# Kernel tuning notes

Measured on AMD Instinct MI355X. Metric: run time of the kernel, lower is better.

Reference implementation:

```python
import jax, jax.numpy as jnp
import numpy as np

HALT_EPS = 0.1
THRESHOLD = 1.0 - HALT_EPS


def setup_inputs() -> dict:
    key = jax.random.key(0)
    ks = jax.random.split(key, 8)
    bsz, seq_len, d, max_hops = 8, 1024, 1024, 6
    d_ff = 4 * d
    inp = {
        "state": jax.random.normal(ks[0], (bsz, seq_len, d), jnp.float32),
        "time_signal": jax.random.normal(ks[1], (1, seq_len, d), jnp.float32) * 0.02,
        "position_signal": jax.random.normal(ks[2], (1, max_hops, d), jnp.float32) * 0.02,
        "w_p": jax.random.normal(ks[3], (d, 1), jnp.float32) * 0.02,
        "b_p": jnp.ones((1,), jnp.float32),  # p.bias.data.fill_(1.0)
        "W1": jax.random.normal(ks[4], (d, d_ff), jnp.float32) * (1.0 / np.sqrt(d)),
        "b1": jnp.zeros((d_ff,), jnp.float32),
        "W2": jax.random.normal(ks[5], (d_ff, d), jnp.float32) * (1.0 / np.sqrt(d_ff)),
        "b2": jnp.zeros((d,), jnp.float32),
        "max_hops": max_hops,
    }
    return inp


def reference(state, time_signal, position_signal, w_p, b_p, W1, b1, W2, b2, max_hops):
    bsz, seq_len, d = state.shape
    dt = state.dtype
    hp = jnp.zeros((bsz, seq_len), dt)   # halting_probability
    rem = jnp.zeros((bsz, seq_len), dt)  # remainders
    nu = jnp.zeros((bsz, seq_len), dt)   # n_updates
    prev = jnp.zeros_like(state)         # previous_state

    def ffn(x):  # transform(): hidden -> 4*hidden -> ReLU -> hidden
        return jax.nn.relu(x @ W1 + b1) @ W2 + b2

    mh = jnp.asarray(max_hops, dt)
    for step in range(max_hops):
        # emulate the data-dependent early break with a scalar gate
        active = jnp.any((hp < THRESHOLD) & (nu < mh))
        s = state + time_signal[:, :seq_len, :]
        s = s + position_signal[:, step, :][:, None, :]
        p = jax.nn.sigmoid(s @ w_p + b_p)[..., 0]  # [bsz, seq_len]
        sr = (hp < 1.0).astype(dt)                 # still_running
        acc = hp + p * sr
        nh = ((acc > THRESHOLD).astype(dt)) * sr   # new_halted
        sr2 = ((acc <= THRESHOLD).astype(dt)) * sr # still_running (updated)
        hp_n = hp + p * sr2
        rem_n = rem + nh * (1.0 - hp_n)
        hp_n = hp_n + nh * rem_n
        nu_n = nu + sr2 + nh
        uw = (p * sr2 + nh * rem_n)[..., None]     # update_weights
        s_t = ffn(s)
        prev_n = s_t * uw + prev * (1.0 - uw)
        # commit only if the torch loop would not have broken yet
        state = jnp.where(active, s_t, state)
        hp = jnp.where(active, hp_n, hp)
        rem = jnp.where(active, rem_n, rem)
        nu = jnp.where(active, nu_n, nu)
        prev = jnp.where(active, prev_n, prev)
    return prev, (rem, nu)
```

## Files before the change

kernel.cpp:

```cpp
#include <hip/hip_runtime.h>
#include <math.h>

typedef unsigned short u16;
typedef unsigned int u32;
typedef __attribute__((ext_vector_type(8))) short short8;
typedef __attribute__((ext_vector_type(4))) float f32x4;
typedef __attribute__((ext_vector_type(4))) u16 u16x4;

#define BSZ 8
#define SEQ 1024
#define DIM 1024
#define DFF 4096
#define MROWS (BSZ * SEQ)
#define HOPS 6

typedef __attribute__((address_space(3))) u32 as3_u32;
typedef __attribute__((address_space(1))) const u32 as1_u32;
#define GLDS(g, l) __builtin_amdgcn_global_load_lds((as1_u32*)(g), (as3_u32*)(l), 16, 0, 0)

__device__ __forceinline__ u16 bf16_rne(float f) {
  u32 u = __float_as_uint(f);
  u32 r = (u + 0x7FFFu + ((u >> 16) & 1u)) >> 16;
  return (u16)r;
}
__device__ __forceinline__ float bf16_to_f(u16 h) {
  return __uint_as_float(((u32)h) << 16);
}

__global__ __launch_bounds__(256)
void tsplit(const float* __restrict__ W, u16* __restrict__ Th, u16* __restrict__ Tl,
            int K, int N) {
  __shared__ float tile[32][33];
  const int n0 = blockIdx.x * 32, k0 = blockIdx.y * 32;
  const int tx = threadIdx.x & 31, ty = threadIdx.x >> 5;
#pragma unroll
  for (int i = 0; i < 4; ++i)
    tile[ty + 8 * i][tx] = W[(long)(k0 + ty + 8 * i) * N + n0 + tx];
  __syncthreads();
#pragma unroll
  for (int i = 0; i < 4; ++i) {
    float v = tile[tx][ty + 8 * i];
    long idx = (long)(n0 + ty + 8 * i) * K + k0 + tx;
    u16 h = bf16_rne(v);
    Th[idx] = h;
    Tl[idx] = bf16_rne(v - bf16_to_f(h));
  }
}

__global__ __launch_bounds__(256)
void s_act(const float* __restrict__ state, const float* __restrict__ ts,
           const float* __restrict__ ps, const float* __restrict__ wp,
           const float* __restrict__ bp,
           u16* __restrict__ sh, u16* __restrict__ sl,
           float* __restrict__ uwp, float* __restrict__ hp,
           float* __restrict__ rem, float* __restrict__ nu) {
  const int row = blockIdx.x;
  const int t = row & (SEQ - 1);
  const int tid = threadIdx.x;
  const long gbase = (long)row * DIM + tid * 4;
  const int dbase = tid * 4;
  f32x4 sv = *(const f32x4*)(state + gbase);
  f32x4 tv = *(const f32x4*)(ts + (long)t * DIM + dbase);
  f32x4 pv = *(const f32x4*)(ps + dbase);
  f32x4 wv = *(const f32x4*)(wp + dbase);
  float dot = 0.f;
  u16x4 hh, llv;
#pragma unroll
  for (int i = 0; i < 4; ++i) {
    float s = sv[i] + tv[i] + pv[i];
    dot += s * wv[i];
    u16 h = bf16_rne(s);
    hh[i] = h;
    llv[i] = bf16_rne(s - bf16_to_f(h));
  }
  *(u16x4*)(sh + gbase) = hh;
  *(u16x4*)(sl + gbase) = llv;
#pragma unroll
  for (int o = 32; o > 0; o >>= 1) dot += __shfl_down(dot, o);
  __shared__ float red[4];
  if ((tid & 63) == 0) red[tid >> 6] = dot;
  __syncthreads();
  if (tid == 0) {
    float z = red[0] + red[1] + red[2] + red[3] + bp[0];
    float p = 1.0f / (1.0f + expf(-z));
    float h = hp[row], r = rem[row], n = nu[row];
    float sr  = (h < 1.0f) ? 1.0f : 0.0f;
    float a   = h + p * sr;
    float nh  = (a > 0.9f) ? sr : 0.0f;
    float sr2 = (a <= 0.9f) ? sr : 0.0f;
    h = h + p * sr2;
    r = r + nh * (1.0f - h);
    h = h + nh * r;
    n = n + sr2 + nh;
    hp[row] = h; rem[row] = r; nu[row] = n;
    uwp[row] = p * sr2 + nh * r;
  }
}

template <int MODE, int NCOLS>
__global__ __launch_bounds__(512, 2)
void gemm8(const u16* __restrict__ aH, const u16* __restrict__ aL,
           const u16* __restrict__ bH, const u16* __restrict__ bL,
           int ldK, int ntPerSplit,
           const float* __restrict__ bias,
           u16* __restrict__ outH, u16* __restrict__ outL,
           float* __restrict__ parts, int Mrows) {
  __shared__ __align__(16) char lds[131072];
  const int tid = threadIdx.x, lane = tid & 63, wave = tid >> 6;
  const int wm = wave >> 2, wn = wave & 3;

  const int gx = gridDim.x, gy = gridDim.y;
  const int nwg = gx * gy * gridDim.z;
  int id = (blockIdx.z * gy + blockIdx.y) * gx + blockIdx.x;
  int swz = (id & 7) * (nwg >> 3) + (id >> 3);
  const int bx = swz % gx;
  int t1 = swz / gx;
  const int by = t1 % gy, bz = t1 / gy;
  const int m0 = by * 256, n0 = bx * 256;
  const int tile0 = bz * ntPerSplit;
  const int NT = ntPerSplit;
  const int niter = NT >> 1;

  const int l8 = lane >> 3, l7 = lane & 7;
  const int lslot = l7 ^ l8;
  u32 rA[2][2], rB[2][2];
#pragma unroll
  for (int hf = 0; hf < 2; ++hf)
#pragma unroll
    for (int g = 0; g < 2; ++g) {
      rA[hf][g] = (u32)(((m0 + hf * 128 + g * 64 + wave * 8 + l8) * ldK + lslot * 8) * 2);
      rB[hf][g] = (u32)(((n0 + hf * 128 + g * 64 + wave * 8 + l8) * ldK + lslot * 8) * 2);
    }

  auto stage = [&](int T, int hf) {
    const int c = T - (T / 3) * 3;
    const int colb = (T / 3) * 128;
    const int buf = T & 1;
    char* ldsb = &lds[buf * 65536 + (hf >= 2 ? 32768 : 0) + (hf & 1) * 16384 + wave * 1024];
    const u16* pl;
    u32 r0b, r1b;
    if (hf < 2) { pl = (c == 2) ? aL : aH; r0b = rA[hf][0]; r1b = rA[hf][1]; }
    else        { pl = (c == 1) ? bL : bH; r0b = rB[hf - 2][0]; r1b = rB[hf - 2][1]; }
    GLDS((const char*)pl + r0b + colb, ldsb);
    GLDS((const char*)pl + r1b + colb, ldsb + 8192);
  };

  const int fr = lane & 15, kg = lane >> 4;
  const int fb2 = (fr >> 2) & 1;
  const int sks[2] = {fb2 << 6, (fb2 ^ 1) << 6};
  const int laneRC = fr * 128 + ((kg ^ (fr & 3)) << 4);
  const int aBaseH = wm * 16384;
  const int bBaseH = 32768 + (wn >> 1) * 16384 + (wn & 1) * 8192;

  f32x4 acc[8][4];
  const f32x4 fz = {0.f, 0.f, 0.f, 0.f};
#pragma unroll
  for (int m = 0; m < 8; ++m)
#pragma unroll
    for (int n = 0; n < 4; ++n) acc[m][n] = fz;

#define LDS8(off) (*(const short8*)&lds[(off)])

  stage(tile0 + 0, 0); stage(tile0 + 0, 1); stage(tile0 + 0, 2); stage(tile0 + 0, 3);
  stage(tile0 + 1, 0);
  asm volatile("s_waitcnt vmcnt(2)" ::: "memory");
  __builtin_amdgcn_s_barrier();

  for (int it = 0; it < niter; ++it) {
#pragma unroll
    for (int ht = 0; ht < 2; ++ht) {
      const int buf = ht;
      const int abase = buf * 65536 + aBaseH;
      const int bbase = buf * 65536 + bBaseH;
      short8 aF[4][2], bF[4][2];
#pragma unroll
      for (int ph = 0; ph < 4; ++ph) {
        if (ph == 0) {
#pragma unroll
          for (int mf = 0; mf < 4; ++mf) {
            aF[mf][0] = LDS8(abase + mf * 2048 + laneRC + sks[0]);
            aF[mf][1] = LDS8(abase + mf * 2048 + laneRC + sks[1]);
          }
#pragma unroll
          for (int nf = 0; nf < 2; ++nf) {
            bF[nf][0] = LDS8(bbase + nf * 2048 + laneRC + sks[0]);
            bF[nf][1] = LDS8(bbase + nf * 2048 + laneRC + sks[1]);
          }
        } else if (ph == 1) {
#pragma unroll
          for (int nf = 2; nf < 4; ++nf) {
            bF[nf][0] = LDS8(bbase + nf * 2048 + laneRC + sks[0]);
            bF[nf][1] = LDS8(bbase + nf * 2048 + laneRC + sks[1]);
          }
        } else if (ph == 2) {
#pragma unroll
          for (int mf = 0; mf < 4; ++mf) {
            aF[mf][0] = LDS8(abase + (4 + mf) * 2048 + laneRC + sks[0]);
            aF[mf][1] = LDS8(abase + (4 + mf) * 2048 + laneRC + sks[1]);
          }
        }
        {
          const int gp = 8 * it + ht * 4 + ph + 1;
          const int T = (gp + 4) >> 2;
          const int hf = (ht * 4 + ph + 5) & 3;
          if (T < NT) stage(tile0 + T, hf);
        }
        __builtin_amdgcn_s_barrier();
        asm volatile("s_waitcnt lgkmcnt(0)" ::: "memory");
        __builtin_amdgcn_s_setprio(1);
        {
          const int qm = ph >> 1, qn = ph & 1;
#pragma unroll
          for (int mm = 0; mm < 4; ++mm)
#pragma unroll
            for (int nn = 0; nn < 2; ++nn) {
              const int mf = qm * 4 + mm, nf = qn * 2 + nn;
              acc[mf][nf] = __builtin_amdgcn_mfma_f32_16x16x32_bf16(aF[mm][0], bF[nf][0], acc[mf][nf], 0, 0, 0);
              acc[mf][nf] = __builtin_amdgcn_mfma_f32_16x16x32_bf16(aF[mm][1], bF[nf][1], acc[mf][nf], 0, 0, 0);
            }
        }
        __builtin_amdgcn_s_setprio(0);
        if (ph == 3) {
          if (it + 1 == niter) { asm volatile("s_waitcnt vmcnt(0)" ::: "memory"); }
          else                 { asm volatile("s_waitcnt vmcnt(2)" ::: "memory"); }
        }
        __builtin_amdgcn_s_barrier();
      }
    }
  }

  const int orow = m0 + wm * 128 + kg * 4;
  const int ocol = n0 + wn * 64 + fr;
#pragma unroll
  for (int mf = 0; mf < 8; ++mf)
#pragma unroll
    for (int nf = 0; nf < 4; ++nf) {
      const int col = ocol + nf * 16;
      if constexpr (MODE == 0) {
        const float bv = bias[col];
#pragma unroll
        for (int i2 = 0; i2 < 4; ++i2) {
          const int row = orow + mf * 16 + i2;
          float v = fmaxf(acc[mf][nf][i2] + bv, 0.f);
          const size_t idx = (size_t)row * NCOLS + col;
          u16 h = bf16_rne(v);
          outH[idx] = h;
          outL[idx] = bf16_rne(v - bf16_to_f(h));
        }
      } else {
        float* pp = parts + (size_t)bz * Mrows * NCOLS;
#pragma unroll
        for (int i2 = 0; i2 < 4; ++i2) {
          const int row = orow + mf * 16 + i2;
          pp[(size_t)row * NCOLS + col] = acc[mf][nf][i2];
        }
      }
    }
#undef LDS8
}

__global__ __launch_bounds__(256)
void combine(const float* __restrict__ parts, long pstride, int nparts,
             const float* __restrict__ b2, const float* __restrict__ uwp,
             float* __restrict__ prev, float* __restrict__ state, int n4) {
  for (int idx = blockIdx.x * blockDim.x + threadIdx.x; idx < n4;
       idx += gridDim.x * blockDim.x) {
    const int row = idx >> 8, c4 = idx & 255;
    f32x4 a = ((const f32x4*)parts)[idx];
    for (int k = 1; k < nparts; ++k) {
      f32x4 b = *(const f32x4*)(parts + (long)k * pstride + (long)idx * 4);
#pragma unroll
      for (int j = 0; j < 4; ++j) a[j] += b[j];
    }
    f32x4 bv = ((const f32x4*)b2)[c4];
    const float u = uwp[row];
    f32x4 pr = ((const f32x4*)prev)[idx];
    f32x4 s, o;
#pragma unroll
    for (int j = 0; j < 4; ++j) {
      s[j] = a[j] + bv[j];
      o[j] = s[j] * u + pr[j] * (1.0f - u);
    }
    ((f32x4*)prev)[idx] = o;
    ((f32x4*)state)[idx] = s;
  }
}

extern "C" void kernel_launch(void* const* d_in, const int* in_sizes, int n_in,
                              void* d_out, int out_size, void* d_ws, size_t ws_size,
                              hipStream_t stream) {
  (void)in_sizes; (void)n_in;
  float* state     = (float*)d_in[0];
  const float* ts  = (const float*)d_in[1];
  const float* ps  = (const float*)d_in[2];
  const float* wp  = (const float*)d_in[3];
  const float* bp  = (const float*)d_in[4];
  const float* W1  = (const float*)d_in[5];
  const float* b1  = (const float*)d_in[6];
  const float* W2  = (const float*)d_in[7];
  const float* b2  = (const float*)d_in[8];

  float* prev = (float*)d_out;
  float* rem  = prev + (size_t)MROWS * DIM;
  float* nu   = rem + MROWS;

  char* base = (char*)d_ws;
  size_t off = 0;
  auto carve = [&](size_t bytes) -> void* {
    void* p = base + off;
    off += (bytes + 255) & ~(size_t)255;
    return p;
  };
  u16* w1h = (u16*)carve((size_t)DFF * DIM * 2);
  u16* w1l = (u16*)carve((size_t)DFF * DIM * 2);
  u16* w2h = (u16*)carve((size_t)DIM * DFF * 2);
  u16* w2l = (u16*)carve((size_t)DIM * DFF * 2);
  u16* sh  = (u16*)carve((size_t)MROWS * DIM * 2);
  u16* sl  = (u16*)carve((size_t)MROWS * DIM * 2);
  float* uwp = (float*)carve((size_t)MROWS * 4);
  float* hp  = (float*)carve((size_t)MROWS * 4);
  const size_t fixed = off;
  int Ms = MROWS;
  while (Ms > 256 && fixed + (size_t)16384 * DIM * 4 + (size_t)Ms * 16384 > ws_size)
    Ms >>= 1;
  u16* hidh    = (u16*)carve((size_t)Ms * DFF * 2);
  u16* hidl    = (u16*)carve((size_t)Ms * DFF * 2);
  float* parts = (float*)carve((size_t)16384 * DIM * 4);
  const int sk = 16384 / Ms;
  const int ntps = 192 / sk;

  hipMemsetAsync(d_out, 0, (size_t)out_size * 4, stream);
  hipMemsetAsync(hp, 0, (size_t)MROWS * 4, stream);

  tsplit<<<dim3(DFF / 32, DIM / 32), 256, 0, stream>>>(W1, w1h, w1l, DIM, DFF);
  tsplit<<<dim3(DIM / 32, DFF / 32), 256, 0, stream>>>(W2, w2h, w2l, DFF, DIM);

  for (int step = 0; step < HOPS; ++step) {
    s_act<<<MROWS, 256, 0, stream>>>(state, ts, ps + (size_t)step * DIM, wp, bp,
                                     sh, sl, uwp, hp, rem, nu);
    for (int r0 = 0; r0 < MROWS; r0 += Ms) {
      gemm8<0, DFF><<<dim3(DFF / 256, Ms / 256, 1), 512, 0, stream>>>(
          sh + (size_t)r0 * DIM, sl + (size_t)r0 * DIM, w1h, w1l,
          DIM, 48, b1, hidh, hidl, nullptr, Ms);
      gemm8<1, DIM><<<dim3(DIM / 256, Ms / 256, sk), 512, 0, stream>>>(
          hidh, hidl, w2h, w2l,
          DFF, ntps, nullptr, nullptr, nullptr, parts, Ms);
      combine<<<2048, 256, 0, stream>>>(
          parts, (long)Ms * DIM, sk, b2, uwp + r0,
          prev + (size_t)r0 * DIM, state + (size_t)r0 * DIM, Ms * 256);
    }
  }
}
```

Baseline: 2.641 ms.

## Fuse combine into next step's activation kernel and add device-side early-exit gates

When the whole batch fits in one chunk, the split-K reduction, bias, previous-state blend and state update are folded into the next hop's s_act kernel. A separate final combine runs once after the last hop. This removes one full-size pass over state and parts per hop. Each kernel also reads a device-side gate flag, set when any row is still running, and returns early if all rows have halted, which emulates the reference's early break without a host sync. The catch is extra atomic loads at kernel entry; with the given inputs, rows may never all halt, so the gates may never skip anything.

```diff
diff --git a/kernel.cpp b/kernel.cpp
--- a/kernel.cpp
+++ b/kernel.cpp
@@ -26,6 +26,9 @@
 __device__ __forceinline__ float bf16_to_f(u16 h) {
   return __uint_as_float(((u32)h) << 16);
 }
+__device__ __forceinline__ int gchk(const int* g) {
+  return g ? __hip_atomic_load(g, __ATOMIC_RELAXED, __HIP_MEMORY_SCOPE_AGENT) : 1;
+}
 
 __global__ __launch_bounds__(256)
 void tsplit(const float* __restrict__ W, u16* __restrict__ Th, u16* __restrict__ Tl,
@@ -47,19 +50,38 @@
   }
 }
 
+template <int NP>
 __global__ __launch_bounds__(256)
-void s_act(const float* __restrict__ state, const float* __restrict__ ts,
-           const float* __restrict__ ps, const float* __restrict__ wp,
-           const float* __restrict__ bp,
-           u16* __restrict__ sh, u16* __restrict__ sl,
-           float* __restrict__ uwp, float* __restrict__ hp,
-           float* __restrict__ rem, float* __restrict__ nu) {
+void s_act_k(const float* __restrict__ src, long pstride,
+             const float* __restrict__ b2, float* __restrict__ prevO,
+             const float* __restrict__ ts, const float* __restrict__ ps,
+             const float* __restrict__ wp, const float* __restrict__ bp,
+             u16* __restrict__ sh, u16* __restrict__ sl,
+             float* __restrict__ uwp, float* __restrict__ hp,
+             float* __restrict__ rem, float* __restrict__ nu,
+             int* __restrict__ gate, int k, const int* __restrict__ gateChk) {
+  if (!gchk(gateChk)) return;
   const int row = blockIdx.x;
   const int t = row & (SEQ - 1);
   const int tid = threadIdx.x;
   const long gbase = (long)row * DIM + tid * 4;
   const int dbase = tid * 4;
-  f32x4 sv = *(const f32x4*)(state + gbase);
+  f32x4 vv;
+  if constexpr (NP == 0) {
+    vv = *(const f32x4*)(src + gbase);
+  } else {
+    f32x4 a = *(const f32x4*)(src + gbase);
+    f32x4 c = *(const f32x4*)(src + pstride + gbase);
+    f32x4 bv = *(const f32x4*)(b2 + dbase);
+#pragma unroll
+    for (int j = 0; j < 4; ++j) vv[j] = a[j] + c[j] + bv[j];
+    const float u = uwp[row];
+    f32x4 pr = *(const f32x4*)(prevO + gbase);
+    f32x4 po;
+#pragma unroll
+    for (int j = 0; j < 4; ++j) po[j] = vv[j] * u + pr[j] * (1.0f - u);
+    *(f32x4*)(prevO + gbase) = po;
+  }
   f32x4 tv = *(const f32x4*)(ts + (long)t * DIM + dbase);
   f32x4 pv = *(const f32x4*)(ps + dbase);
   f32x4 wv = *(const f32x4*)(wp + dbase);
@@ -67,7 +89,7 @@
   u16x4 hh, llv;
 #pragma unroll
   for (int i = 0; i < 4; ++i) {
-    float s = sv[i] + tv[i] + pv[i];
+    float s = vv[i] + tv[i] + pv[i];
     dot += s * wv[i];
     u16 h = bf16_rne(s);
     hh[i] = h;
@@ -85,6 +107,8 @@
     float p = 1.0f / (1.0f + expf(-z));
     float h = hp[row], r = rem[row], n = nu[row];
     float sr  = (h < 1.0f) ? 1.0f : 0.0f;
+    if (sr > 0.0f)
+      __hip_atomic_store(&gate[k], 1, __ATOMIC_RELAXED, __HIP_MEMORY_SCOPE_AGENT);
     float a   = h + p * sr;
     float nh  = (a > 0.9f) ? sr : 0.0f;
     float sr2 = (a <= 0.9f) ? sr : 0.0f;
@@ -104,7 +128,8 @@
            int ldK, int ntPerSplit,
            const float* __restrict__ bias,
            u16* __restrict__ outH, u16* __restrict__ outL,
-           float* __restrict__ parts, int Mrows) {
+           float* __restrict__ parts, int Mrows, const int* __restrict__ gate) {
+  if (!gchk(gate)) return;
   __shared__ __align__(16) char lds[131072];
   const int tid = threadIdx.x, lane = tid & 63, wave = tid >> 6;
   const int wm = wave >> 2, wn = wave & 3;
@@ -260,9 +285,31 @@
 }
 
 __global__ __launch_bounds__(256)
+void combineF(const float* __restrict__ parts, long pstride,
+              const float* __restrict__ b2, const float* __restrict__ uwp,
+              float* __restrict__ prev, int n4, const int* __restrict__ gateChk) {
+  if (!gchk(gateChk)) return;
+  for (int idx = blockIdx.x * blockDim.x + threadIdx.x; idx < n4;
+       idx += gridDim.x * blockDim.x) {
+    const int row = idx >> 8, c4 = idx & 255;
+    f32x4 a = ((const f32x4*)parts)[idx];
+    f32x4 b = *(const f32x4*)(parts + pstride + (long)idx * 4);
+    f32x4 bv = ((const f32x4*)b2)[c4];
+    const float u = uwp[row];
+    f32x4 pr = ((const f32x4*)prev)[idx];
+    f32x4 o;
+#pragma unroll
+    for (int j = 0; j < 4; ++j) o[j] = (a[j] + b[j] + bv[j]) * u + pr[j] * (1.0f - u);
+    ((f32x4*)prev)[idx] = o;
+  }
+}
+
+__global__ __launch_bounds__(256)
 void combine(const float* __restrict__ parts, long pstride, int nparts,
              const float* __restrict__ b2, const float* __restrict__ uwp,
-             float* __restrict__ prev, float* __restrict__ state, int n4) {
+             float* __restrict__ prev, float* __restrict__ state, int n4,
+             const int* __restrict__ gateChk) {
+  if (!gchk(gateChk)) return;
   for (int idx = blockIdx.x * blockDim.x + threadIdx.x; idx < n4;
        idx += gridDim.x * blockDim.x) {
     const int row = idx >> 8, c4 = idx & 255;
@@ -319,6 +366,7 @@
   u16* sl  = (u16*)carve((size_t)MROWS * DIM * 2);
   float* uwp = (float*)carve((size_t)MROWS * 4);
   float* hp  = (float*)carve((size_t)MROWS * 4);
+  int* gate  = (int*)carve(256);
   const size_t fixed = off;
   int Ms = MROWS;
   while (Ms > 256 && fixed + (size_t)16384 * DIM * 4 + (size_t)Ms * 16384 > ws_size)
@@ -328,26 +376,48 @@
   float* parts = (float*)carve((size_t)16384 * DIM * 4);
   const int sk = 16384 / Ms;
   const int ntps = 192 / sk;
+  const bool fused = (Ms == MROWS);
 
   hipMemsetAsync(d_out, 0, (size_t)out_size * 4, stream);
-  hipMemsetAsync(hp, 0, (size_t)MROWS * 4, stream);
+  hipMemsetAsync(hp, 0, (size_t)MROWS * 4 + 256, stream);
 
   tsplit<<<dim3(DFF / 32, DIM / 32), 256, 0, stream>>>(W1, w1h, w1l, DIM, DFF);
   tsplit<<<dim3(DIM / 32, DFF / 32), 256, 0, stream>>>(W2, w2h, w2l, DFF, DIM);
 
   for (int step = 0; step < HOPS; ++step) {
-    s_act<<<MROWS, 256, 0, stream>>>(state, ts, ps + (size_t)step * DIM, wp, bp,
-                                     sh, sl, uwp, hp, rem, nu);
-    for (int r0 = 0; r0 < MROWS; r0 += Ms) {
-      gemm8<0, DFF><<<dim3(DFF / 256, Ms / 256, 1), 512, 0, stream>>>(
-          sh + (size_t)r0 * DIM, sl + (size_t)r0 * DIM, w1h, w1l,
-          DIM, 48, b1, hidh, hidl, nullptr, Ms);
-      gemm8<1, DIM><<<dim3(DIM / 256, Ms / 256, sk), 512, 0, stream>>>(
-          hidh, hidl, w2h, w2l,
-          DFF, ntps, nullptr, nullptr, nullptr, parts, Ms);
-      combine<<<2048, 256, 0, stream>>>(
-          parts, (long)Ms * DIM, sk, b2, uwp + r0,
-          prev + (size_t)r0 * DIM, state + (size_t)r0 * DIM, Ms * 256);
-    }
-  }
-}
+    const int* gPrev = step ? &gate[step - 1] : nullptr;
+    if (fused) {
+      if (step == 0)
+        s_act_k<0><<<MROWS, 256, 0, stream>>>(
+            state, 0, nullptr, nullptr, ts, ps + (size_t)step * DIM, wp, bp,
+            sh, sl, uwp, hp, rem, nu, gate, step, nullptr);
+      else
+        s_act_k<2><<<MROWS, 256, 0, stream>>>(
+            parts, (long)MROWS * DIM, b2, prev, ts, ps + (size_t)step * DIM, wp, bp,
+            sh, sl, uwp, hp, rem, nu, gate, step, gPrev);
+      gemm8<0, DFF><<<dim3(DFF / 256, MROWS / 256, 1), 512, 0, stream>>>(
+          sh, sl, w1h, w1l, DIM, 48, b1, hidh, hidl, nullptr, MROWS, &gate[step]);
+      gemm8<1, DIM><<<dim3(DIM / 256, MROWS / 256, 2), 512, 0, stream>>>(
+          hidh, hidl, w2h, w2l, DFF, 96, nullptr, nullptr, nullptr, parts, MROWS,
+          &gate[step]);
+    } else {
+      s_act_k<0><<<MROWS, 256, 0, stream>>>(
+          state, 0, nullptr, nullptr, ts, ps + (size_t)step * DIM, wp, bp,
+          sh, sl, uwp, hp, rem, nu, gate, step, gPrev);
+      for (int r0 = 0; r0 < MROWS; r0 += Ms) {
+        gemm8<0, DFF><<<dim3(DFF / 256, Ms / 256, 1), 512, 0, stream>>>(
+            sh + (size_t)r0 * DIM, sl + (size_t)r0 * DIM, w1h, w1l,
+            DIM, 48, b1, hidh, hidl, nullptr, Ms, &gate[step]);
+        gemm8<1, DIM><<<dim3(DIM / 256, Ms / 256, sk), 512, 0, stream>>>(
+            hidh, hidl, w2h, w2l, DFF, ntps, nullptr, nullptr, nullptr, parts, Ms,
+            &gate[step]);
+        combine<<<2048, 256, 0, stream>>>(
+            parts, (long)Ms * DIM, sk, b2, uwp + r0,
+            prev + (size_t)r0 * DIM, state + (size_t)r0 * DIM, Ms * 256, &gate[step]);
+      }
+    }
+  }
+  if (fused)
+    combineF<<<2048, 256, 0, stream>>>(parts, (long)MROWS * DIM, b2, uwp, prev,
+                                       MROWS * 256, &gate[HOPS - 1]);
+}
```

Result: faster. 2.129 ms (-19.4%).
